# Optimization experiments

Hardware: AMD Instinct MI355X
Metric: run time of the kernel (lower is better)

Reference implementation:

```python
import jax, jax.numpy as jnp
import numpy as np

D = 300      # dim_in (hardcoded in HGConv)
N_CAT = 3    # n_categories
M = 16384    # nodes
E = 4096     # hyperedges


def setup_inputs() -> dict:
    key = jax.random.key(0)
    ks = jax.random.split(key, 11)
    s = 1.0 / np.sqrt(D)
    u = lambda k, shape: jax.random.uniform(k, shape, jnp.float32, -s, s)
    return {
        "node_feats": jax.random.normal(ks[0], (M, D), jnp.float32),
        "edge_feats": jax.random.normal(ks[1], (E, D), jnp.float32),
        "inc_mat": jax.random.uniform(ks[2], (M, E), jnp.float32),
        # VertexConv params (Linear weights stored as (in, out); torch stores transpose)
        "W_att": u(ks[3], (D, D)),       # attention, no bias
        "W_proj": u(ks[4], (D, D)),      # projection, no bias
        "alpha": jnp.array(0.5, jnp.float32),
        # HypergraphEdgeAggregation params
        "ec_W_att": u(ks[5], (D, 1)),    # attention, no bias
        "ec_W_proj": u(ks[6], (D, D)),
        "ec_b_proj": u(ks[7], (D,)),
        # final classifier
        "fc_W": u(ks[8], (D, N_CAT)),
        "fc_b": u(ks[9], (N_CAT,)),
    }


def reference(node_feats, edge_feats, inc_mat, W_att, W_proj, alpha,
              ec_W_att, ec_W_proj, ec_b_proj, fc_W, fc_b):
    # --- VertexConv ---
    # edge attention scores: inc^T @ (X @ W_att)  -> (e, d)
    edge_att = inc_mat.T @ (node_feats @ W_att)
    attn = jax.nn.softmax(edge_att, axis=1)
    # fused equivalent of einsum('me,md->med') then einsum('med,ed->ed'):
    # edge_feat[e,d] = (inc^T @ X)[e,d] * attn[e,d]
    ef = (inc_mat.T @ node_feats) * attn
    ef = ef @ W_proj
    ef = alpha * edge_feats + (1.0 - alpha) * ef          # residual mix
    # --- HypergraphEdgeAggregation ---
    scores = ef @ ec_W_att                                # (e, 1)
    w = jax.nn.softmax(scores, axis=0)                    # softmax over edges
    pooled = jnp.sum(ef * w, axis=0)                      # (d,)
    out = pooled @ ec_W_proj + ec_b_proj                  # (d,)
    # --- classifier (LogSoftmax is defined but NOT applied in forward) ---
    logits = out @ fc_W + fc_b                            # (n_categories,)
    return logits
```

## Files before the change

### kernel.cpp

```cpp
#include <hip/hip_runtime.h>
#include <math.h>

typedef _Float16 f16;
typedef _Float16 f16x8 __attribute__((ext_vector_type(8)));
typedef _Float16 f16x4 __attribute__((ext_vector_type(4)));
typedef __fp16 fp16x2 __attribute__((ext_vector_type(2)));
typedef float f32x4 __attribute__((ext_vector_type(4)));
typedef float f32x16 __attribute__((ext_vector_type(16)));

#define NM 16384
#define NE 4096
#define ND 300
#define DP 320
#define PS 1310720

#define GLOAD_LDS16(gsrc, ldst)                                              \
  __builtin_amdgcn_global_load_lds(                                          \
      (__attribute__((address_space(1))) void*)(gsrc),                       \
      (__attribute__((address_space(3))) void*)(ldst), 16, 0, 0)

#define K2WAIT(N) asm volatile("s_waitcnt vmcnt(" #N ") lgkmcnt(0)" ::: "memory")
#define K2BAR()                                        \
  do {                                                 \
    asm volatile("" ::: "memory");                     \
    __builtin_amdgcn_s_barrier();                      \
    asm volatile("" ::: "memory");                     \
  } while (0)
#define K2BARW()                                       \
  do {                                                 \
    asm volatile("s_waitcnt lgkmcnt(0)" ::: "memory"); \
    __builtin_amdgcn_s_barrier();                      \
    asm volatile("" ::: "memory");                     \
  } while (0)

__global__ __launch_bounds__(256) void k01_prep(const float* __restrict__ X,
                                                const float* __restrict__ Watt,
                                                f16* __restrict__ XT,
                                                f16* __restrict__ WT) {
  __shared__ f16 tile[64][324];
  const int bx = blockIdx.x;
  if (bx < 256) {
    int m0 = bx * 64;
    for (int idx = threadIdx.x; idx < 64 * 80; idx += 256) {
      int m = idx / 80, q = idx % 80;
      int d = q * 4;
      float4 v = make_float4(0.f, 0.f, 0.f, 0.f);
      if (d < ND) v = *(const float4*)(X + (size_t)(m0 + m) * ND + d);
      tile[m][d] = (f16)v.x; tile[m][d + 1] = (f16)v.y;
      tile[m][d + 2] = (f16)v.z; tile[m][d + 3] = (f16)v.w;
    }
    __syncthreads();
    for (int idx = threadIdx.x; idx < DP * 8; idx += 256) {
      int d = idx >> 3, part = idx & 7;
      f16x8 hv;
#pragma unroll
      for (int i = 0; i < 8; ++i) hv[i] = tile[part * 8 + i][d];
      *(f16x8*)(XT + (size_t)d * NM + m0 + part * 8) = hv;
    }
  } else {
    int idx = (bx - 256) * 256 + threadIdx.x;
    if (idx < DP * DP) {
      int j = idx / DP, d = idx % DP;
      float v = (j < ND && d < ND) ? Watt[d * ND + j] : 0.f;
      WT[(size_t)j * DP + d] = (f16)v;
    }
  }
}

__global__ __launch_bounds__(256, 2) void k2_bigmm(const float* __restrict__ inc,
                                                   const f16* __restrict__ XT,
                                                   f16* __restrict__ Zp) {
  __shared__ __align__(16) char lds[77824];
  const int t = threadIdx.x, lane = t & 63, wid = t >> 6;
  const int bx = blockIdx.x;
  const int kb = (bx & 7) | (((bx >> 3) & 1) << 3);
  const int eb = bx >> 4;
  const int e0 = eb * 128;
  const size_t kbase = (size_t)kb * 1024;
  f16* __restrict__ Zout = Zp + (size_t)kb * PS;

  const int we = wid >> 1, wj = wid & 1;
  const int l31 = lane & 31, oct = lane >> 5;
  int sl[2];
#pragma unroll
  for (int kk = 0; kk < 2; ++kk)
    sl[kk] = (((kk * 2 + oct) ^ ((l31 >> 1) & 3)) & 3) << 4;
  const int arow = (we * 64 + l31) * 64;
  const int brow = (wj * 160 + l31) * 64;
  const int ep = t & 63, kq = t >> 6;
  const int sA = (kq ^ (ep & 3)) & 3;
  const int wa0 = 61440 + ep * 128 + sA * 16;
  const float* pA = inc + (kbase + kq * 8) * NE + e0 + 2 * ep;
  const int br = wid * 80 + (lane >> 2);
  const f16* pB = XT + (size_t)br * NM + kbase + 8 * ((lane & 3) ^ ((lane >> 3) & 3));

  float2 rA0[8], rA1[8];
  f32x16 acc[2][5];
#pragma unroll
  for (int me = 0; me < 2; ++me)
#pragma unroll
    for (int f = 0; f < 5; ++f)
#pragma unroll
      for (int r = 0; r < 16; ++r) acc[me][f][r] = 0.f;

#define LOADA(R)                                                               \
  {                                                                            \
    _Pragma("unroll") for (int i = 0; i < 8; ++i)                              \
        R[i] = *(const float2*)(pA + (size_t)i * NE);                          \
    pA += (size_t)32 * NE;                                                     \
  }
#define DMAB(S)                                                                \
  {                                                                            \
    _Pragma("unroll") for (int i = 0; i < 5; ++i) {                            \
      GLOAD_LDS16(pB + (size_t)(i * 16) * NM,                                  \
                  lds + (S)*20480 + wid * 5120 + i * 1024);                    \
    }                                                                          \
    pB += 32;                                                                  \
  }
#define WRITEA(R, S)                                                           \
  {                                                                            \
    union { fp16x2 h; uint32_t u; } ux_[4], uy_[4];                            \
    _Pragma("unroll") for (int z = 0; z < 4; ++z) {                            \
      ux_[z].h = __builtin_amdgcn_cvt_pkrtz(R[2 * z].x, R[2 * z + 1].x);       \
      uy_[z].h = __builtin_amdgcn_cvt_pkrtz(R[2 * z].y, R[2 * z + 1].y);       \
    }                                                                          \
    *(uint4*)(lds + wa0 + (S)*8192) =                                          \
        make_uint4(ux_[0].u, ux_[1].u, ux_[2].u, ux_[3].u);                    \
    *(uint4*)(lds + wa0 + 64 + (S)*8192) =                                     \
        make_uint4(uy_[0].u, uy_[1].u, uy_[2].u, uy_[3].u);                    \
  }
#define COMPUTE(BS, AS)                                                        \
  {                                                                            \
    __builtin_amdgcn_s_setprio(1);                                             \
    _Pragma("unroll") for (int kk = 0; kk < 2; ++kk) {                         \
      f16x8 a0_ = *(const f16x8*)(lds + 61440 + (AS)*8192 + arow + sl[kk]);    \
      f16x8 a1_ = *(const f16x8*)(lds + 61440 + (AS)*8192 + arow + 2048 + sl[kk]); \
      _Pragma("unroll") for (int f = 0; f < 5; ++f) {                          \
        f16x8 b_ = *(const f16x8*)(lds + (BS)*20480 + brow + f * 2048 + sl[kk]); \
        acc[0][f] = __builtin_amdgcn_mfma_f32_32x32x16_f16(a0_, b_, acc[0][f], 0, 0, 0); \
        acc[1][f] = __builtin_amdgcn_mfma_f32_32x32x16_f16(a1_, b_, acc[1][f], 0, 0, 0); \
      }                                                                        \
    }                                                                          \
    __builtin_amdgcn_s_setprio(0);                                             \
  }
#define BODY(BSTG, BCMP, AW, AC, RL, RW)                                       \
  DMAB(BSTG);                                                                  \
  LOADA(RL);                                                                   \
  WRITEA(RW, AW); \
  K2BARW();                                                                    \
  COMPUTE(BCMP, AC);                                                           \
  K2BAR();

  LOADA(rA0);
  DMAB(0);
  WRITEA(rA0, 0);
  LOADA(rA1);
  DMAB(1);
  BODY(2, 0, 1, 0, rA0, rA1);

  for (int it = 0; it < 4; ++it) {
    BODY(0, 1, 0, 1, rA1, rA0);
    BODY(1, 2, 1, 0, rA0, rA1);
    BODY(2, 0, 0, 1, rA1, rA0);
    BODY(0, 1, 1, 0, rA0, rA1);
    BODY(1, 2, 0, 1, rA1, rA0);
    BODY(2, 0, 1, 0, rA0, rA1);
  }
  BODY(0, 1, 0, 1, rA1, rA0);
  BODY(1, 2, 1, 0, rA0, rA1);
  BODY(2, 0, 0, 1, rA1, rA0);
  BODY(0, 1, 1, 0, rA0, rA1);
  BODY(1, 2, 0, 1, rA1, rA0);
  WRITEA(rA1, 1);
  K2WAIT(0);
  K2BAR();
  COMPUTE(0, 0);
  K2BAR();
  COMPUTE(1, 1);

#pragma unroll
  for (int me = 0; me < 2; ++me)
#pragma unroll
    for (int f = 0; f < 5; ++f) {
      int jg = wj * 160 + f * 32 + l31;
      int ebase = e0 + we * 64 + me * 32 + 4 * oct;
#pragma unroll
      for (int r = 0; r < 16; ++r) {
        int eg = ebase + (r & 3) + 8 * (r >> 2);
        Zout[(size_t)eg * DP + jg] = (f16)acc[me][f][r];
      }
    }
#undef LOADA
#undef DMAB
#undef WRITEA
#undef COMPUTE
#undef BODY
}

__global__ __launch_bounds__(256, 1) void k2bs_att(const f16* __restrict__ Zp,
                                                   const f16* __restrict__ WT,
                                                   f16* __restrict__ EF0,
                                                   float* __restrict__ att) {
  __shared__ __align__(16) char lds[49152];
  const int t = threadIdx.x, lane = t & 63, wid = t >> 6;
  const int e0 = blockIdx.x * 64;
  {
    const size_t base = (size_t)e0 * DP;
    for (int i = t; i < 2560; i += 256) {
      size_t idx = base + (size_t)i * 8;
      float s[8];
#pragma unroll
      for (int z = 0; z < 8; ++z) s[z] = 0.f;
#pragma unroll
      for (int p = 0; p < 16; ++p) {
        f16x8 v = *(const f16x8*)(Zp + (size_t)p * PS + idx);
#pragma unroll
        for (int z = 0; z < 8; ++z) s[z] += (float)v[z];
      }
      f16x8 o;
#pragma unroll
      for (int z = 0; z < 8; ++z) o[z] = (f16)s[z];
      *(f16x8*)(EF0 + idx) = o;
    }
    asm volatile("s_waitcnt vmcnt(0)" ::: "memory");
    __syncthreads();
  }
  const int we = wid >> 1, wj = wid & 1;
  const int l31 = lane & 31, oct = lane >> 5;
  int sl[2];
#pragma unroll
  for (int kk = 0; kk < 2; ++kk)
    sl[kk] = (((kk * 2 + oct) ^ ((l31 >> 1) & 3)) & 3) << 4;
  const int arow = (we * 32 + l31) * 64;
  const int brow = (wj * 160 + l31) * 64;
  const int srcsw = 8 * ((lane & 3) ^ ((lane >> 3) & 3));
  const f16* pA = EF0 + (size_t)(e0 + wid * 16 + (lane >> 2)) * DP + srcsw;
  const f16* pB = WT + (size_t)(wid * 80 + (lane >> 2)) * DP + srcsw;

  f32x16 acc[5];
#pragma unroll
  for (int f = 0; f < 5; ++f)
#pragma unroll
    for (int r = 0; r < 16; ++r) acc[f][r] = 0.f;

#define STAGE2(S)                                                              \
  {                                                                            \
    GLOAD_LDS16(pA, lds + 40960 + (S)*4096 + wid * 1024);                      \
    pA += 32;                                                                  \
    _Pragma("unroll") for (int i = 0; i < 5; ++i) {                            \
      GLOAD_LDS16(pB + (size_t)(i * 16) * DP,                                  \
                  lds + (S)*20480 + wid * 5120 + i * 1024);                    \
    }                                                                          \
    pB += 32;                                                                  \
  }
#define COMPUTE2(S)                                                            \
  {                                                                            \
    _Pragma("unroll") for (int kk = 0; kk < 2; ++kk) {                         \
      f16x8 a_ = *(const f16x8*)(lds + 40960 + (S)*4096 + arow + sl[kk]);      \
      _Pragma("unroll") for (int f = 0; f < 5; ++f) {                          \
        f16x8 b_ = *(const f16x8*)(lds + (S)*20480 + brow + f * 2048 + sl[kk]); \
        acc[f] = __builtin_amdgcn_mfma_f32_32x32x16_f16(a_, b_, acc[f], 0, 0, 0); \
      }                                                                        \
    }                                                                          \
  }

  STAGE2(0);
  STAGE2(1);
  K2WAIT(6);
  K2BAR();
  for (int tt = 0; tt < 8; ++tt) {
    COMPUTE2(tt & 1);
    K2BAR();
    STAGE2(tt & 1);
    K2WAIT(6);
    K2BAR();
  }
  COMPUTE2(0);
  K2BAR();
  K2WAIT(0);
  COMPUTE2(1);

#pragma unroll
  for (int f = 0; f < 5; ++f) {
    int jg = wj * 160 + f * 32 + l31;
    int ebase = e0 + we * 32 + 4 * oct;
#pragma unroll
    for (int r = 0; r < 16; ++r) {
      int eg = ebase + (r & 3) + 8 * (r >> 2);
      att[(size_t)eg * DP + jg] = acc[f][r];
    }
  }
#undef STAGE2
#undef COMPUTE2
}

__global__ __launch_bounds__(256) void k3_edge(const float* __restrict__ att,
                                               const f16* __restrict__ EF0,
                                               const float* __restrict__ edge_feats,
                                               const float* __restrict__ Wproj,
                                               const float* __restrict__ alphaP,
                                               const float* __restrict__ ecWatt,
                                               float* __restrict__ ef,
                                               float* __restrict__ scores) {
  __shared__ float efw[16][304];
  const int t = threadIdx.x, lane = t & 63, w = t >> 6;
  const int e0 = blockIdx.x * 16;
  for (int el = 0; el < 4; ++el) {
    int e = e0 + w * 4 + el;
    const size_t ro = (size_t)e * DP;
    float p[5];
    float mx = -1e30f;
#pragma unroll
    for (int u = 0; u < 5; ++u) {
      int d = u * 64 + lane;
      p[u] = (d < ND) ? att[ro + d] : -1e30f;
      mx = fmaxf(mx, p[u]);
    }
    for (int o = 32; o; o >>= 1) mx = fmaxf(mx, __shfl_xor(mx, o));
    float s = 0.f;
#pragma unroll
    for (int u = 0; u < 5; ++u) {
      int d = u * 64 + lane;
      float pe = (d < ND) ? expf(p[u] - mx) : 0.f;
      p[u] = pe;
      s += pe;
    }
    for (int o = 32; o; o >>= 1) s += __shfl_xor(s, o);
    float inv = 1.f / s;
#pragma unroll
    for (int u = 0; u < 5; ++u) {
      int d = u * 64 + lane;
      if (d < 304)
        efw[w * 4 + el][d] = (d < ND) ? (float)EF0[ro + d] * p[u] * inv : 0.f;
    }
  }
  __syncthreads();
  const int jl = lane & 15, kc = lane >> 4;
  const float alpha = alphaP[0];
  float acc[4][19];
#pragma unroll
  for (int ei = 0; ei < 4; ++ei)
#pragma unroll
    for (int jj = 0; jj < 19; ++jj) acc[ei][jj] = 0.f;
  const int d0 = kc * 75;
  const float* efw0 = &efw[w * 4 + 0][0];
  const float* efw1 = &efw[w * 4 + 1][0];
  const float* efw2 = &efw[w * 4 + 2][0];
  const float* efw3 = &efw[w * 4 + 3][0];
  for (int dd = 0; dd < 75; ++dd) {
    int d = d0 + dd;
    const float* wr = Wproj + (size_t)d * ND + jl;
    float w0 = efw0[d], w1 = efw1[d], w2 = efw2[d], w3 = efw3[d];
#pragma unroll
    for (int jj = 0; jj < 19; ++jj) {
      int j = jl + jj * 16;
      float wv = (j < ND) ? wr[jj * 16] : 0.f;
      acc[0][jj] += w0 * wv;
      acc[1][jj] += w1 * wv;
      acc[2][jj] += w2 * wv;
      acc[3][jj] += w3 * wv;
    }
  }
#pragma unroll
  for (int ei = 0; ei < 4; ++ei)
#pragma unroll
    for (int jj = 0; jj < 19; ++jj) {
      acc[ei][jj] += __shfl_xor(acc[ei][jj], 16);
      acc[ei][jj] += __shfl_xor(acc[ei][jj], 32);
    }
  float scp[4] = {0.f, 0.f, 0.f, 0.f};
#pragma unroll
  for (int ei = 0; ei < 4; ++ei) {
    int e = e0 + w * 4 + ei;
#pragma unroll
    for (int jj = 0; jj < 19; ++jj) {
      int j = jl + jj * 16;
      float v = 0.f;
      if (j < ND) {
        v = alpha * edge_feats[(size_t)e * ND + j] + (1.f - alpha) * acc[ei][jj];
        scp[ei] += v * ecWatt[j];
      }
      if (kc == 0) ef[(size_t)e * 304 + j] = v;
    }
  }
#pragma unroll
  for (int ei = 0; ei < 4; ++ei)
    for (int o = 8; o; o >>= 1) scp[ei] += __shfl_xor(scp[ei], o);
  if (lane == 0) {
#pragma unroll
    for (int ei = 0; ei < 4; ++ei) scores[e0 + w * 4 + ei] = scp[ei];
  }
}

__global__ __launch_bounds__(256) void k4ab_pool(const float* __restrict__ sc,
                                                 const float* __restrict__ ef,
                                                 float* __restrict__ pp) {
  __shared__ float redm[4];
  __shared__ float reds[4];
  __shared__ float wsh[64];
  const int t = threadIdx.x, lane = t & 63, w = t >> 6;
  float v[16];
  float mx = -1e30f;
#pragma unroll
  for (int u = 0; u < 16; ++u) {
    v[u] = sc[t + u * 256];
    mx = fmaxf(mx, v[u]);
  }
  for (int o = 32; o; o >>= 1) mx = fmaxf(mx, __shfl_xor(mx, o));
  if (lane == 0) redm[w] = mx;
  __syncthreads();
  float m2 = fmaxf(fmaxf(redm[0], redm[1]), fmaxf(redm[2], redm[3]));
  float s = 0.f;
#pragma unroll
  for (int u = 0; u < 16; ++u) s += expf(v[u] - m2);
  for (int o = 32; o; o >>= 1) s += __shfl_xor(s, o);
  if (lane == 0) reds[w] = s;
  __syncthreads();
  float inv = 1.f / (reds[0] + reds[1] + reds[2] + reds[3]);
  const int e0 = blockIdx.x * 64;
  if (t < 64) wsh[t] = expf(sc[e0 + t] - m2) * inv;
  __syncthreads();
  for (int j = t; j < 304; j += 256) {
    float acc = 0.f;
#pragma unroll 8
    for (int e = 0; e < 64; ++e) acc += wsh[e] * ef[(size_t)(e0 + e) * 304 + j];
    pp[blockIdx.x * 304 + j] = acc;
  }
}

__global__ __launch_bounds__(320) void k4c_final(const float* __restrict__ pp,
                                                 const float* __restrict__ ecWp,
                                                 const float* __restrict__ ecb,
                                                 const float* __restrict__ fcW,
                                                 const float* __restrict__ fcb,
                                                 float* __restrict__ out) {
  __shared__ float pooled[304];
  __shared__ float o[304];
  const int t = threadIdx.x;
  if (t < 304) {
    float acc = 0.f;
#pragma unroll 8
    for (int b = 0; b < 64; ++b) acc += pp[b * 304 + t];
    pooled[t] = acc;
  }
  __syncthreads();
  if (t < ND) {
    float acc = ecb[t];
#pragma unroll 4
    for (int j = 0; j < ND; ++j) acc += pooled[j] * ecWp[(size_t)j * ND + t];
    o[t] = acc;
  }
  __syncthreads();
  if (t < 64) {
#pragma unroll
    for (int c = 0; c < 3; ++c) {
      float a = 0.f;
      for (int j2 = t; j2 < ND; j2 += 64) a += o[j2] * fcW[j2 * 3 + c];
      for (int off = 32; off; off >>= 1) a += __shfl_xor(a, off);
      if (t == 0) out[c] = a + fcb[c];
    }
  }
}

extern "C" void kernel_launch(void* const* d_in, const int* in_sizes, int n_in,
                              void* d_out, int out_size, void* d_ws, size_t ws_size,
                              hipStream_t stream) {
  const float* X = (const float*)d_in[0];
  const float* EFEATS = (const float*)d_in[1];
  const float* INC = (const float*)d_in[2];
  const float* WATT = (const float*)d_in[3];
  const float* WPROJ = (const float*)d_in[4];
  const float* ALPHA = (const float*)d_in[5];
  const float* ECATT = (const float*)d_in[6];
  const float* ECWP = (const float*)d_in[7];
  const float* ECB = (const float*)d_in[8];
  const float* FCW = (const float*)d_in[9];
  const float* FCB = (const float*)d_in[10];

  char* ws = (char*)d_ws;
  f16* XT = (f16*)(ws);
  f16* Zp = (f16*)(ws + 10485760);
  f16* WT = (f16*)(ws + 52428800);
  f16* EF0 = (f16*)(ws + 52633600);
  float* att = (float*)(ws + 55255040);
  float* ef = (float*)(ws + 60497920);
  float* sc = (float*)(ws + 65478656);
  float* pp = (float*)(ws + 65495040);

  hipLaunchKernelGGL(k01_prep, dim3(656), dim3(256), 0, stream, X, WATT, XT, WT);
  hipLaunchKernelGGL(k2_bigmm, dim3(512), dim3(256), 0, stream, INC, XT, Zp);
  hipLaunchKernelGGL(k2bs_att, dim3(64), dim3(256), 0, stream, Zp, WT, EF0, att);
  hipLaunchKernelGGL(k3_edge, dim3(256), dim3(256), 0, stream, att, EF0, EFEATS,
                     WPROJ, ALPHA, ECATT, ef, sc);
  hipLaunchKernelGGL(k4ab_pool, dim3(64), dim3(256), 0, stream, sc, ef, pp);
  hipLaunchKernelGGL(k4c_final, dim3(1), dim3(320), 0, stream, pp, ECWP, ECB, FCW,
                     FCB, (float*)d_out);
}
```

Baseline: 242.6 us.

## Use 512-thread blocks in big matmul and split partial-sum reduction into own kernel

The main incidence-matrix GEMM now runs 8 waves per block, each computing a 32-row slice instead of 64 rows, which halves per-wave accumulator registers and changes how A and B tiles are loaded into LDS. The 16-way split-K partial-sum reduction moves out of the attention GEMM kernel into a separate 640-block kernel, so the reduction is spread over many more blocks instead of 64. This adds one extra kernel launch and a global round trip for EF0, and each wave does less MFMA work per LDS fetch.

```diff
diff --git a/kernel.cpp b/kernel.cpp
--- a/kernel.cpp
+++ b/kernel.cpp
@@ -67,7 +67,7 @@
   }
 }
 
-__global__ __launch_bounds__(256, 2) void k2_bigmm(const float* __restrict__ inc,
+__global__ __launch_bounds__(512, 2) void k2_bigmm(const float* __restrict__ inc,
                                                    const f16* __restrict__ XT,
                                                    f16* __restrict__ Zp) {
   __shared__ __align__(16) char lds[77824];
@@ -85,60 +85,51 @@
 #pragma unroll
   for (int kk = 0; kk < 2; ++kk)
     sl[kk] = (((kk * 2 + oct) ^ ((l31 >> 1) & 3)) & 3) << 4;
-  const int arow = (we * 64 + l31) * 64;
+  const int arow = (we * 32 + l31) * 64;
   const int brow = (wj * 160 + l31) * 64;
-  const int ep = t & 63, kq = t >> 6;
-  const int sA = (kq ^ (ep & 3)) & 3;
-  const int wa0 = 61440 + ep * 128 + sA * 16;
-  const float* pA = inc + (kbase + kq * 8) * NE + e0 + 2 * ep;
-  const int br = wid * 80 + (lane >> 2);
-  const f16* pB = XT + (size_t)br * NM + kbase + 8 * ((lane & 3) ^ ((lane >> 3) & 3));
-
-  float2 rA0[8], rA1[8];
-  f32x16 acc[2][5];
-#pragma unroll
-  for (int me = 0; me < 2; ++me)
-#pragma unroll
-    for (int f = 0; f < 5; ++f)
-#pragma unroll
-      for (int r = 0; r < 16; ++r) acc[me][f][r] = 0.f;
+  const int ae = t & 127, kq = t >> 7;
+  const int wa = 61440 + ae * 64 + (((kq ^ ((ae >> 1) & 3)) & 3) << 4);
+  const float* pA = inc + (kbase + kq * 8) * NE + e0 + ae;
+  const int bsw = 8 * ((lane & 3) ^ ((lane >> 3) & 3));
+  const f16* pB0 = XT + (size_t)(wid * 16 + (lane >> 2)) * NM + kbase + bsw;
+  const f16* pB1 = XT + (size_t)((8 + wid) * 16 + (lane >> 2)) * NM + kbase + bsw;
+  const f16* pB2 = XT + (size_t)((16 + wid) * 16 + (lane >> 2)) * NM + kbase + bsw;
+
+  float rA0[8], rA1[8];
+  f32x16 acc[5];
+#pragma unroll
+  for (int f = 0; f < 5; ++f)
+#pragma unroll
+    for (int r = 0; r < 16; ++r) acc[f][r] = 0.f;
 
 #define LOADA(R)                                                               \
   {                                                                            \
     _Pragma("unroll") for (int i = 0; i < 8; ++i)                              \
-        R[i] = *(const float2*)(pA + (size_t)i * NE);                          \
+        R[i] = pA[(size_t)i * NE];                                             \
     pA += (size_t)32 * NE;                                                     \
   }
 #define DMAB(S)                                                                \
   {                                                                            \
-    _Pragma("unroll") for (int i = 0; i < 5; ++i) {                            \
-      GLOAD_LDS16(pB + (size_t)(i * 16) * NM,                                  \
-                  lds + (S)*20480 + wid * 5120 + i * 1024);                    \
-    }                                                                          \
-    pB += 32;                                                                  \
+    GLOAD_LDS16(pB0, lds + (S)*20480 + wid * 1024);                            \
+    GLOAD_LDS16(pB1, lds + (S)*20480 + (8 + wid) * 1024);                      \
+    if (wid < 4) GLOAD_LDS16(pB2, lds + (S)*20480 + (16 + wid) * 1024);        \
+    pB0 += 32; pB1 += 32; pB2 += 32;                                           \
   }
 #define WRITEA(R, S)                                                           \
   {                                                                            \
-    union { fp16x2 h; uint32_t u; } ux_[4], uy_[4];                            \
-    _Pragma("unroll") for (int z = 0; z < 4; ++z) {                            \
-      ux_[z].h = __builtin_amdgcn_cvt_pkrtz(R[2 * z].x, R[2 * z + 1].x);       \
-      uy_[z].h = __builtin_amdgcn_cvt_pkrtz(R[2 * z].y, R[2 * z + 1].y);       \
-    }                                                                          \
-    *(uint4*)(lds + wa0 + (S)*8192) =                                          \
-        make_uint4(ux_[0].u, ux_[1].u, ux_[2].u, ux_[3].u);                    \
-    *(uint4*)(lds + wa0 + 64 + (S)*8192) =                                     \
-        make_uint4(uy_[0].u, uy_[1].u, uy_[2].u, uy_[3].u);                    \
+    union { fp16x2 h; uint32_t u; } u_[4];                                     \
+    _Pragma("unroll") for (int z = 0; z < 4; ++z)                              \
+      u_[z].h = __builtin_amdgcn_cvt_pkrtz(R[2 * z], R[2 * z + 1]);            \
+    *(uint4*)(lds + wa + (S)*8192) = make_uint4(u_[0].u, u_[1].u, u_[2].u, u_[3].u); \
   }
 #define COMPUTE(BS, AS)                                                        \
   {                                                                            \
     __builtin_amdgcn_s_setprio(1);                                             \
     _Pragma("unroll") for (int kk = 0; kk < 2; ++kk) {                         \
-      f16x8 a0_ = *(const f16x8*)(lds + 61440 + (AS)*8192 + arow + sl[kk]);    \
-      f16x8 a1_ = *(const f16x8*)(lds + 61440 + (AS)*8192 + arow + 2048 + sl[kk]); \
+      f16x8 a_ = *(const f16x8*)(lds + 61440 + (AS)*8192 + arow + sl[kk]);     \
       _Pragma("unroll") for (int f = 0; f < 5; ++f) {                          \
         f16x8 b_ = *(const f16x8*)(lds + (BS)*20480 + brow + f * 2048 + sl[kk]); \
-        acc[0][f] = __builtin_amdgcn_mfma_f32_32x32x16_f16(a0_, b_, acc[0][f], 0, 0, 0); \
-        acc[1][f] = __builtin_amdgcn_mfma_f32_32x32x16_f16(a1_, b_, acc[1][f], 0, 0, 0); \
+        acc[f] = __builtin_amdgcn_mfma_f32_32x32x16_f16(a_, b_, acc[f], 0, 0, 0); \
       }                                                                        \
     }                                                                          \
     __builtin_amdgcn_s_setprio(0);                                             \
@@ -179,17 +170,15 @@
   COMPUTE(1, 1);
 
 #pragma unroll
-  for (int me = 0; me < 2; ++me)
-#pragma unroll
-    for (int f = 0; f < 5; ++f) {
-      int jg = wj * 160 + f * 32 + l31;
-      int ebase = e0 + we * 64 + me * 32 + 4 * oct;
-#pragma unroll
-      for (int r = 0; r < 16; ++r) {
-        int eg = ebase + (r & 3) + 8 * (r >> 2);
-        Zout[(size_t)eg * DP + jg] = (f16)acc[me][f][r];
-      }
-    }
+  for (int f = 0; f < 5; ++f) {
+    int jg = wj * 160 + f * 32 + l31;
+    int ebase = e0 + we * 32 + 4 * oct;
+#pragma unroll
+    for (int r = 0; r < 16; ++r) {
+      int eg = ebase + (r & 3) + 8 * (r >> 2);
+      Zout[(size_t)eg * DP + jg] = (f16)acc[f][r];
+    }
+  }
 #undef LOADA
 #undef DMAB
 #undef WRITEA
@@ -197,34 +186,30 @@
 #undef BODY
 }
 
-__global__ __launch_bounds__(256, 1) void k2bs_att(const f16* __restrict__ Zp,
-                                                   const f16* __restrict__ WT,
-                                                   f16* __restrict__ EF0,
-                                                   float* __restrict__ att) {
+__global__ __launch_bounds__(256) void k2s_sum(const f16* __restrict__ Zp,
+                                               f16* __restrict__ EF0) {
+  const size_t idx = ((size_t)blockIdx.x * 256 + threadIdx.x) * 8;
+  float s[8];
+#pragma unroll
+  for (int z = 0; z < 8; ++z) s[z] = 0.f;
+#pragma unroll
+  for (int p = 0; p < 16; ++p) {
+    f16x8 v = *(const f16x8*)(Zp + (size_t)p * PS + idx);
+#pragma unroll
+    for (int z = 0; z < 8; ++z) s[z] += (float)v[z];
+  }
+  f16x8 o;
+#pragma unroll
+  for (int z = 0; z < 8; ++z) o[z] = (f16)s[z];
+  *(f16x8*)(EF0 + idx) = o;
+}
+
+__global__ __launch_bounds__(256, 1) void k2b_att(const f16* __restrict__ EF0,
+                                                  const f16* __restrict__ WT,
+                                                  float* __restrict__ att) {
   __shared__ __align__(16) char lds[49152];
   const int t = threadIdx.x, lane = t & 63, wid = t >> 6;
   const int e0 = blockIdx.x * 64;
-  {
-    const size_t base = (size_t)e0 * DP;
-    for (int i = t; i < 2560; i += 256) {
-      size_t idx = base + (size_t)i * 8;
-      float s[8];
-#pragma unroll
-      for (int z = 0; z < 8; ++z) s[z] = 0.f;
-#pragma unroll
-      for (int p = 0; p < 16; ++p) {
-        f16x8 v = *(const f16x8*)(Zp + (size_t)p * PS + idx);
-#pragma unroll
-        for (int z = 0; z < 8; ++z) s[z] += (float)v[z];
-      }
-      f16x8 o;
-#pragma unroll
-      for (int z = 0; z < 8; ++z) o[z] = (f16)s[z];
-      *(f16x8*)(EF0 + idx) = o;
-    }
-    asm volatile("s_waitcnt vmcnt(0)" ::: "memory");
-    __syncthreads();
-  }
   const int we = wid >> 1, wj = wid & 1;
   const int l31 = lane & 31, oct = lane >> 5;
   int sl[2];
@@ -488,8 +473,9 @@
   float* pp = (float*)(ws + 65495040);
 
   hipLaunchKernelGGL(k01_prep, dim3(656), dim3(256), 0, stream, X, WATT, XT, WT);
-  hipLaunchKernelGGL(k2_bigmm, dim3(512), dim3(256), 0, stream, INC, XT, Zp);
-  hipLaunchKernelGGL(k2bs_att, dim3(64), dim3(256), 0, stream, Zp, WT, EF0, att);
+  hipLaunchKernelGGL(k2_bigmm, dim3(512), dim3(512), 0, stream, INC, XT, Zp);
+  hipLaunchKernelGGL(k2s_sum, dim3(640), dim3(256), 0, stream, Zp, EF0);
+  hipLaunchKernelGGL(k2b_att, dim3(64), dim3(256), 0, stream, EF0, WT, att);
   hipLaunchKernelGGL(k3_edge, dim3(256), dim3(256), 0, stream, att, EF0, EFEATS,
                      WPROJ, ALPHA, ECATT, ef, sc);
   hipLaunchKernelGGL(k4ab_pool, dim3(64), dim3(256), 0, stream, sc, ef, pp);
```

After: 262.3 us. +8.1%, slower.
